# Performance work log

Hardware: AMD Instinct MI355X
Metric: run time of the kernel (lower is better)

## Reference

```python
import jax, jax.numpy as jnp
import numpy as np

N_ENT = 50000
N_REL = 200
N_EDGE = 1_000_000
D = 64


def setup_inputs() -> dict:
    key = jax.random.key(0)
    ks = jax.random.split(key, 12)
    src = jax.random.randint(ks[0], (N_EDGE,), 0, N_ENT)
    rel = jax.random.randint(ks[1], (N_EDGE,), 0, N_REL)
    dst = jax.random.randint(ks[2], (N_EDGE,), 0, N_ENT)
    triples = jnp.stack([src, rel, dst], axis=1).astype(jnp.int64)  # [E,3]
    s = 1.0 / np.sqrt(D)
    return {
        "emb_e": jax.random.normal(ks[3], (N_ENT, D), jnp.float32) * s,
        "re_att": jax.random.normal(ks[4], (N_REL,), jnp.float32) * 0.1,
        "W1": jax.random.normal(ks[5], (D, D), jnp.float32) * s,
        "W2": jax.random.normal(ks[6], (D, D), jnp.float32) * s,
        "W3": jax.random.normal(ks[7], (D, D), jnp.float32) * s,
        "u": jax.random.normal(ks[8], (3 * D,), jnp.float32) * s,
        "en_weight": jax.random.normal(ks[9], (D, D), jnp.float32) * s,
        "re_weight": jax.random.normal(ks[10], (D, D), jnp.float32) * s,
        "re_spec": jax.random.normal(ks[11], (D,), jnp.float32) * s,
        "triples": triples,
    }


def _forward(emb_e, re_att, W1, W2, W3, u, en_weight, re_weight, re_spec, triples):
    src = triples[:, 0]
    rel = triples[:, 1]
    dst = triples[:, 2]
    n = emb_e.shape[0]

    def wgc(x, W):
        # relation-weighted message passing: out[s] += w[r] * x[d]
        msg = jax.ops.segment_sum(x[dst] * re_att[rel][:, None], src, num_segments=n)
        return jnp.tanh((x + msg) @ W)

    x = wgc(emb_e, W1)
    x = wgc(x, W2)
    x = wgc(x, W3)

    # GAT-style edge scores: e = LeakyReLU(u . [W_en h_i ; W_re r_spec ; W_en h_j])
    d = x.shape[1]
    hs = x @ en_weight.T                       # [N,d] = (en_weight @ h)^T rows
    z_src = hs @ u[:d]                         # [N]
    z_dst = hs @ u[2 * d:]                     # [N]
    z_mid = u[d:2 * d] @ (re_weight @ re_spec)  # scalar, same for every edge
    scores = jax.nn.leaky_relu(z_src[src] + z_mid + z_dst[dst], 0.01)  # [E]

    # softmax normalized over ALL triples (global denominator, per source code)
    alpha = jax.nn.softmax(scores)

    # out[src] += alpha_e * x[dst]
    out = jax.ops.segment_sum(alpha[:, None] * x[dst], src, num_segments=n)
    return out


def reference(emb_e, re_att, W1, W2, W3, u, en_weight, re_weight, re_spec, triples):
    return _forward(emb_e, re_att, W1, W2, W3, u, en_weight, re_weight, re_spec, triples)
```

## Files before the change

### kernel.cpp

```cpp
#include <hip/hip_runtime.h>
#include <math.h>

#define N_ENT  50000
#define N_REL  200
#define N_EDGE 1000000
#define CHUNK  196
#define ECH    7813
#define NRNG   6250

#define WS_MISC   0
#define WS_ZSUM   128
#define WS_ZMID   192
#define WS_A      256
#define WS_B      512
#define WS_BSUM   0x000E0000
#define WS_BBASE  0x000F0000
#define WS_COUNTS 0x00100000
#define WS_OFFS   0x00140000
#define WS_ZSRC   0x00180000
#define WS_ZDST   0x001C0000
#define WS_SNODE  0x00200000
#define WS_EPK    0x00240000
#define WS_PACKED 0x00640000
#define WS_SRCS   0x00A40000
#define WS_RANK   0x00E40000
#define WS_XB1    0x00A40000
#define WS_XB0    0x01240000

__device__ __forceinline__ float bflo(unsigned u) { return __uint_as_float(u << 16); }
__device__ __forceinline__ float bfhi(unsigned u) { return __uint_as_float(u & 0xffff0000u); }
__device__ __forceinline__ unsigned short f2bf(float f) {
  unsigned u = __float_as_uint(f);
  unsigned r = ((u >> 16) & 1u) + 0x7fffu;
  return (unsigned short)((u + r) >> 16);
}
__device__ __forceinline__ float lanebc(float v, int k) {
  return __uint_as_float((unsigned)__builtin_amdgcn_readlane((int)__float_as_uint(v), k));
}
__device__ __forceinline__ float fast_tanh(float x) {
  float ex = __expf(2.f * x);
  return 1.f - __fdividef(2.f, ex + 1.f);
}
__device__ __forceinline__ void fma8(float* acc, float wt, uint4 q) {
  acc[0] += wt * bflo(q.x); acc[1] += wt * bfhi(q.x);
  acc[2] += wt * bflo(q.y); acc[3] += wt * bfhi(q.y);
  acc[4] += wt * bflo(q.z); acc[5] += wt * bfhi(q.z);
  acc[6] += wt * bflo(q.w); acc[7] += wt * bfhi(q.w);
}

__global__ void k_init(const void* tri, int* counts, int* misc, double* zsum) {
  int i = blockIdx.x * blockDim.x + threadIdx.x;
  if (i < N_ENT) counts[i] = 0;
  if (blockIdx.x == 0 && threadIdx.x < 64) {
    int l = threadIdx.x;
    int z = ((const int*)tri)[2 * l + 1];
    unsigned long long m = __ballot(z == 0);
    if (l == 0) { misc[0] = (m == ~0ull) ? 1 : 0; *zsum = 0.0; }
  }
}

__global__ void k_conv(const float* __restrict__ x, unsigned short* __restrict__ xb) {
  int i = blockIdx.x * blockDim.x + threadIdx.x;
  if (i >= N_ENT * 16) return;
  float4 v = ((const float4*)x)[i];
  ushort4 o;
  o.x = f2bf(v.x); o.y = f2bf(v.y); o.z = f2bf(v.z); o.w = f2bf(v.w);
  ((ushort4*)xb)[i] = o;
}

__global__ void k_decode(const void* tri, int* __restrict__ counts,
                         int* __restrict__ srcs, unsigned* __restrict__ packed,
                         int* __restrict__ rank, const int* misc) {
  int is64 = misc[0];
  int stride = gridDim.x * blockDim.x;
  if (is64) {
    const long long* t = (const long long*)tri;
    for (int e = blockIdx.x * blockDim.x + threadIdx.x; e < N_EDGE; e += stride) {
      int s = (int)t[3 * e], r = (int)t[3 * e + 1], d = (int)t[3 * e + 2];
      srcs[e] = s;
      packed[e] = ((unsigned)r << 16) | (unsigned)d;
      rank[e] = atomicAdd(&counts[s], 1);
    }
  } else {
    const int* t = (const int*)tri;
    for (int e = blockIdx.x * blockDim.x + threadIdx.x; e < N_EDGE; e += stride) {
      int s = t[3 * e], r = t[3 * e + 1], d = t[3 * e + 2];
      srcs[e] = s;
      packed[e] = ((unsigned)r << 16) | (unsigned)d;
      rank[e] = atomicAdd(&counts[s], 1);
    }
  }
}

__global__ void k_scanA(const int* __restrict__ counts, int* __restrict__ bsum) {
  __shared__ int sm[4];
  int t = threadIdx.x;
  int i = blockIdx.x * CHUNK + t;
  int v = (t < CHUNK && i < N_ENT) ? counts[i] : 0;
  for (int o = 32; o; o >>= 1) v += __shfl_down(v, o);
  if ((t & 63) == 0) sm[t >> 6] = v;
  __syncthreads();
  if (t == 0) bsum[blockIdx.x] = sm[0] + sm[1] + sm[2] + sm[3];
}

__global__ void k_scanB(const int* __restrict__ bsum, int* __restrict__ bbase, int* __restrict__ offs) {
  __shared__ int sm[256];
  int t = threadIdx.x;
  int v = bsum[t];
  sm[t] = v;
  __syncthreads();
  for (int d = 1; d < 256; d <<= 1) {
    int x = (t >= d) ? sm[t - d] : 0;
    __syncthreads();
    sm[t] += x;
    __syncthreads();
  }
  bbase[t] = sm[t] - v;
  if (t == 255) offs[N_ENT] = sm[255];
}

__global__ void k_scanC(const int* __restrict__ counts, const int* __restrict__ bbase,
                        int* __restrict__ offs) {
  __shared__ int sm[256];
  int t = threadIdx.x;
  int i = blockIdx.x * CHUNK + t;
  int v = (t < CHUNK && i < N_ENT) ? counts[i] : 0;
  sm[t] = v;
  __syncthreads();
  for (int d = 1; d < 256; d <<= 1) {
    int x = (t >= d) ? sm[t - d] : 0;
    __syncthreads();
    sm[t] += x;
    __syncthreads();
  }
  if (t < CHUNK && i < N_ENT)
    offs[i] = bbase[blockIdx.x] + sm[t] - v;
}

__global__ void k_scatter(const int* __restrict__ srcs, const int* __restrict__ rank,
                          const unsigned* __restrict__ packed, const int* __restrict__ offs,
                          unsigned* __restrict__ epk) {
  int q = blockIdx.x >> 3, x = blockIdx.x & 7;
  int lo = q * ECH, hi = lo + ECH;
  if (hi > N_EDGE) hi = N_EDGE;
  for (int e = lo + threadIdx.x; e < hi; e += 256) {
    int s = srcs[e];
    if (s / NRNG == x)
      epk[offs[s] + rank[e]] = packed[e];
  }
}

__global__ void k_pre(const float* u, const float* enw, const float* rew, const float* rsp,
                      float* a, float* b, float* zmid) {
  int k = threadIdx.x;
  float aa = 0.f, bb = 0.f;
  for (int j = 0; j < 64; j++) {
    float w = enw[j * 64 + k];
    aa += u[j] * w;
    bb += u[128 + j] * w;
  }
  a[k] = aa; b[k] = bb;
  float t = 0.f;
  for (int c = 0; c < 64; c++) t += rew[k * 64 + c] * rsp[c];
  t *= u[64 + k];
  for (int o = 32; o; o >>= 1) t += __shfl_down(t, o);
  if (k == 0) *zmid = t;
}

template <int EPI>
__global__ void __launch_bounds__(256) k_wgc(
    const unsigned short* __restrict__ xb, const float* __restrict__ W,
    const int* __restrict__ offs, const unsigned* __restrict__ epk,
    const float* __restrict__ re_att, unsigned short* __restrict__ yb,
    const float* __restrict__ a, const float* __restrict__ b,
    float* __restrict__ zsrc, float* __restrict__ zdst) {
  __shared__ float s_att[N_REL];
  for (int t = threadIdx.x; t < N_REL; t += 256) s_att[t] = re_att[t];
  __syncthreads();
  int wid = (blockIdx.x * blockDim.x + threadIdx.x) >> 6;
  int lane = threadIdx.x & 63;
  if (wid >= N_ENT) return;
  int node = wid;
  int g = lane >> 3, c8 = (lane & 7) * 8;
  int e0 = offs[node], e1 = offs[node + 1];
  float acc[8] = {0.f, 0.f, 0.f, 0.f, 0.f, 0.f, 0.f, 0.f};
  {
    uint4 q = *(const uint4*)(xb + (size_t)node * 64 + c8);
    fma8(acc, (g == 0) ? 1.f : 0.f, q);
  }
  for (int e = e0; e < e1; e += 16) {
    int ia = e + g, ib = ia + 8;
    bool va = ia < e1, vb = ib < e1;
    unsigned pa = epk[va ? ia : e0];
    unsigned pb = epk[vb ? ib : e0];
    float wa = va ? s_att[pa >> 16] : 0.f;
    float wb = vb ? s_att[pb >> 16] : 0.f;
    uint4 qa = *(const uint4*)(xb + (size_t)(pa & 0xffffu) * 64 + c8);
    uint4 qb = *(const uint4*)(xb + (size_t)(pb & 0xffffu) * 64 + c8);
    fma8(acc, wa, qa);
    fma8(acc, wb, qb);
  }
#pragma unroll
  for (int off = 8; off <= 32; off <<= 1)
#pragma unroll
    for (int c = 0; c < 8; c++) acc[c] += __shfl_xor(acc[c], off);
  float o = 0.f;
#pragma unroll
  for (int j = 0; j < 8; j++)
#pragma unroll
    for (int c = 0; c < 8; c++)
      o += lanebc(acc[c], j) * W[(j * 8 + c) * 64 + lane];
  float yv = fast_tanh(o);
  yb[(size_t)node * 64 + lane] = f2bf(yv);
  if (EPI) {
    float za = yv * a[lane], zb = yv * b[lane];
    for (int s = 32; s; s >>= 1) { za += __shfl_down(za, s); zb += __shfl_down(zb, s); }
    if (lane == 0) { zsrc[node] = za; zdst[node] = zb; }
  }
}

__global__ void __launch_bounds__(256) k_out(
    const unsigned short* __restrict__ xb, const int* __restrict__ offs,
    const unsigned* __restrict__ epk, const float* __restrict__ zs,
    const float* __restrict__ zd, const float* zmid,
    float* __restrict__ out, float* __restrict__ snode) {
  int wid = (blockIdx.x * blockDim.x + threadIdx.x) >> 6;
  int lane = threadIdx.x & 63;
  if (wid >= N_ENT) return;
  int node = wid;
  int g = lane >> 3, c8 = (lane & 7) * 8;
  float zi = zs[node] + *zmid;
  float acc[8] = {0.f, 0.f, 0.f, 0.f, 0.f, 0.f, 0.f, 0.f};
  float s0 = 0.f;
  int e0 = offs[node], e1 = offs[node + 1];
  for (int e = e0; e < e1; e += 16) {
    int ia = e + g, ib = ia + 8;
    bool va = ia < e1, vb = ib < e1;
    unsigned pa = epk[va ? ia : e0];
    unsigned pb = epk[vb ? ib : e0];
    int da = pa & 0xffffu, db = pb & 0xffffu;
    float ca = zi + zd[da];
    float cb = zi + zd[db];
    ca = ca >= 0.f ? ca : 0.01f * ca;
    cb = cb >= 0.f ? cb : 0.01f * cb;
    float wa = va ? __expf(ca) : 0.f;
    float wb = vb ? __expf(cb) : 0.f;
    uint4 qa = *(const uint4*)(xb + (size_t)da * 64 + c8);
    uint4 qb = *(const uint4*)(xb + (size_t)db * 64 + c8);
    fma8(acc, wa, qa);
    fma8(acc, wb, qb);
    s0 += wa + wb;
  }
#pragma unroll
  for (int off = 8; off <= 32; off <<= 1) {
#pragma unroll
    for (int c = 0; c < 8; c++) acc[c] += __shfl_xor(acc[c], off);
    s0 += __shfl_xor(s0, off);
  }
  if (lane < 8) {
    float4* p = (float4*)(out + (size_t)node * 64 + lane * 8);
    p[0] = make_float4(acc[0], acc[1], acc[2], acc[3]);
    p[1] = make_float4(acc[4], acc[5], acc[6], acc[7]);
  }
  if (lane == 0) snode[node] = s0;
}

__global__ void k_red(const float* __restrict__ snode, double* zsum) {
  int stride = gridDim.x * blockDim.x;
  double s = 0.0;
  for (int i = blockIdx.x * blockDim.x + threadIdx.x; i < N_ENT; i += stride)
    s += (double)snode[i];
  for (int o = 32; o; o >>= 1) s += __shfl_down(s, o);
  __shared__ double ws_[4];
  if ((threadIdx.x & 63) == 0) ws_[threadIdx.x >> 6] = s;
  __syncthreads();
  if (threadIdx.x == 0)
    atomicAdd(zsum, ws_[0] + ws_[1] + ws_[2] + ws_[3]);
}

__global__ void k_norm(float* __restrict__ out, const double* zsum) {
  int i = blockIdx.x * blockDim.x + threadIdx.x;
  if (i >= N_ENT * 16) return;
  float invZ = (float)(1.0 / *zsum);
  float4 v = ((float4*)out)[i];
  v.x *= invZ; v.y *= invZ; v.z *= invZ; v.w *= invZ;
  ((float4*)out)[i] = v;
}

extern "C" void kernel_launch(void* const* d_in, const int* in_sizes, int n_in,
                              void* d_out, int out_size, void* d_ws, size_t ws_size,
                              hipStream_t stream) {
  const float* emb   = (const float*)d_in[0];
  const float* reatt = (const float*)d_in[1];
  const float* W1    = (const float*)d_in[2];
  const float* W2    = (const float*)d_in[3];
  const float* W3    = (const float*)d_in[4];
  const float* u     = (const float*)d_in[5];
  const float* enw   = (const float*)d_in[6];
  const float* rew   = (const float*)d_in[7];
  const float* rsp   = (const float*)d_in[8];
  const void*  tri   = d_in[9];

  char* ws = (char*)d_ws;
  int*            misc   = (int*)(ws + WS_MISC);
  double*         zsum   = (double*)(ws + WS_ZSUM);
  float*          zmid   = (float*)(ws + WS_ZMID);
  float*          a      = (float*)(ws + WS_A);
  float*          b      = (float*)(ws + WS_B);
  int*            bsum   = (int*)(ws + WS_BSUM);
  int*            bbase  = (int*)(ws + WS_BBASE);
  int*            counts = (int*)(ws + WS_COUNTS);
  int*            offs   = (int*)(ws + WS_OFFS);
  float*          zsrc   = (float*)(ws + WS_ZSRC);
  float*          zdst   = (float*)(ws + WS_ZDST);
  float*          snode  = (float*)(ws + WS_SNODE);
  unsigned*       epk    = (unsigned*)(ws + WS_EPK);
  unsigned*       packed = (unsigned*)(ws + WS_PACKED);
  int*            srcs   = (int*)(ws + WS_SRCS);
  int*            rank   = (int*)(ws + WS_RANK);
  unsigned short* xb0    = (unsigned short*)(ws + WS_XB0);
  unsigned short* xb1    = (unsigned short*)(ws + WS_XB1);
  float*          out    = (float*)d_out;

  k_init<<<196, 256, 0, stream>>>(tri, counts, misc, zsum);
  k_conv<<<3125, 256, 0, stream>>>(emb, xb0);
  k_decode<<<1024, 256, 0, stream>>>(tri, counts, srcs, packed, rank, misc);
  k_scanA<<<256, 256, 0, stream>>>(counts, bsum);
  k_scanB<<<1, 256, 0, stream>>>(bsum, bbase, offs);
  k_scanC<<<256, 256, 0, stream>>>(counts, bbase, offs);
  k_scatter<<<1024, 256, 0, stream>>>(srcs, rank, packed, offs, epk);
  k_pre<<<1, 64, 0, stream>>>(u, enw, rew, rsp, a, b, zmid);

  int nb = (N_ENT * 64 + 255) / 256;
  k_wgc<0><<<nb, 256, 0, stream>>>(xb0, W1, offs, epk, reatt, xb1, nullptr, nullptr, nullptr, nullptr);
  k_wgc<0><<<nb, 256, 0, stream>>>(xb1, W2, offs, epk, reatt, xb0, nullptr, nullptr, nullptr, nullptr);
  k_wgc<1><<<nb, 256, 0, stream>>>(xb0, W3, offs, epk, reatt, xb1, a, b, zsrc, zdst);

  k_out<<<nb, 256, 0, stream>>>(xb1, offs, epk, zsrc, zdst, zmid, out, snode);
  k_red<<<196, 256, 0, stream>>>(snode, zsum);
  k_norm<<<3125, 256, 0, stream>>>(out, zsum);
}
```

Measured before the change: 247.2 us.

## Replicate per-source counters eightfold to cut atomic contention in CSR build

Edge decoding now spreads its per-source atomic counters across 8 replicas chosen by block index, and packs src, replica and rank into one word. This reduces the three per-edge arrays to two. A new merge kernel turns the replica counts into per-replica base offsets and totals, which feed the existing scan. The scatter then uses offs + rbase + rank to place each edge. The aim is less atomic contention and less intermediate memory traffic, at the cost of an extra kernel, 8x larger counter init, and a rank field limited to 13 bits.

```diff
diff --git a/kernel.cpp b/kernel.cpp
--- a/kernel.cpp
+++ b/kernel.cpp
@@ -11,19 +11,20 @@
 #define WS_MISC   0
 #define WS_ZSUM   128
 #define WS_ZMID   192
-#define WS_A      256
-#define WS_B      512
+#define WS_AV     256
+#define WS_BV     512
 #define WS_BSUM   0x000E0000
 #define WS_BBASE  0x000F0000
-#define WS_COUNTS 0x00100000
-#define WS_OFFS   0x00140000
-#define WS_ZSRC   0x00180000
-#define WS_ZDST   0x001C0000
-#define WS_SNODE  0x00200000
-#define WS_EPK    0x00240000
-#define WS_PACKED 0x00640000
-#define WS_SRCS   0x00A40000
-#define WS_RANK   0x00E40000
+#define WS_CNT8   0x00100000
+#define WS_RBASE  0x00300000
+#define WS_TOT    0x00500000
+#define WS_OFFS   0x00540000
+#define WS_ZSRC   0x00580000
+#define WS_ZDST   0x005C0000
+#define WS_SNODE  0x00600000
+#define WS_EPK    0x00640000
+#define WS_EA     0x00A40000
+#define WS_EB     0x00E40000
 #define WS_XB1    0x00A40000
 #define WS_XB0    0x01240000
 
@@ -48,9 +49,9 @@
   acc[6] += wt * bflo(q.w); acc[7] += wt * bfhi(q.w);
 }
 
-__global__ void k_init(const void* tri, int* counts, int* misc, double* zsum) {
+__global__ void k_init(const void* tri, int* cnt8, int* misc, double* zsum) {
   int i = blockIdx.x * blockDim.x + threadIdx.x;
-  if (i < N_ENT) counts[i] = 0;
+  if (i < 8 * N_ENT) cnt8[i] = 0;
   if (blockIdx.x == 0 && threadIdx.x < 64) {
     int l = threadIdx.x;
     int z = ((const int*)tri)[2 * l + 1];
@@ -68,28 +69,42 @@
   ((ushort4*)xb)[i] = o;
 }
 
-__global__ void k_decode(const void* tri, int* __restrict__ counts,
-                         int* __restrict__ srcs, unsigned* __restrict__ packed,
-                         int* __restrict__ rank, const int* misc) {
+__global__ void k_decode(const void* tri, int* __restrict__ cnt8,
+                         unsigned* __restrict__ ea, unsigned* __restrict__ eb,
+                         const int* misc) {
   int is64 = misc[0];
+  int rep = blockIdx.x & 7;
   int stride = gridDim.x * blockDim.x;
   if (is64) {
     const long long* t = (const long long*)tri;
     for (int e = blockIdx.x * blockDim.x + threadIdx.x; e < N_EDGE; e += stride) {
       int s = (int)t[3 * e], r = (int)t[3 * e + 1], d = (int)t[3 * e + 2];
-      srcs[e] = s;
-      packed[e] = ((unsigned)r << 16) | (unsigned)d;
-      rank[e] = atomicAdd(&counts[s], 1);
+      int rk = atomicAdd(&cnt8[rep * N_ENT + s], 1);
+      ea[e] = ((unsigned)s << 16) | ((unsigned)rep << 13) | (unsigned)rk;
+      eb[e] = ((unsigned)r << 16) | (unsigned)d;
     }
   } else {
     const int* t = (const int*)tri;
     for (int e = blockIdx.x * blockDim.x + threadIdx.x; e < N_EDGE; e += stride) {
       int s = t[3 * e], r = t[3 * e + 1], d = t[3 * e + 2];
-      srcs[e] = s;
-      packed[e] = ((unsigned)r << 16) | (unsigned)d;
-      rank[e] = atomicAdd(&counts[s], 1);
+      int rk = atomicAdd(&cnt8[rep * N_ENT + s], 1);
+      ea[e] = ((unsigned)s << 16) | ((unsigned)rep << 13) | (unsigned)rk;
+      eb[e] = ((unsigned)r << 16) | (unsigned)d;
     }
   }
+}
+
+__global__ void k_merge(const int* __restrict__ cnt8, int* __restrict__ rbase,
+                        int* __restrict__ tot) {
+  int s = blockIdx.x * blockDim.x + threadIdx.x;
+  if (s >= N_ENT) return;
+  int run = 0;
+#pragma unroll
+  for (int rep = 0; rep < 8; rep++) {
+    rbase[rep * N_ENT + s] = run;
+    run += cnt8[rep * N_ENT + s];
+  }
+  tot[s] = run;
 }
 
 __global__ void k_scanA(const int* __restrict__ counts, int* __restrict__ bsum) {
@@ -137,16 +152,20 @@
     offs[i] = bbase[blockIdx.x] + sm[t] - v;
 }
 
-__global__ void k_scatter(const int* __restrict__ srcs, const int* __restrict__ rank,
-                          const unsigned* __restrict__ packed, const int* __restrict__ offs,
+__global__ void k_scatter(const unsigned* __restrict__ ea, const unsigned* __restrict__ eb,
+                          const int* __restrict__ offs, const int* __restrict__ rbase,
                           unsigned* __restrict__ epk) {
   int q = blockIdx.x >> 3, x = blockIdx.x & 7;
   int lo = q * ECH, hi = lo + ECH;
   if (hi > N_EDGE) hi = N_EDGE;
   for (int e = lo + threadIdx.x; e < hi; e += 256) {
-    int s = srcs[e];
-    if (s / NRNG == x)
-      epk[offs[s] + rank[e]] = packed[e];
+    unsigned a = ea[e];
+    int s = a >> 16;
+    if (s / NRNG == x) {
+      int rep = (a >> 13) & 7;
+      int rk = a & 8191;
+      epk[offs[s] + rbase[rep * N_ENT + s] + rk] = eb[e];
+    }
   }
 }
 
@@ -305,36 +324,38 @@
   int*            misc   = (int*)(ws + WS_MISC);
   double*         zsum   = (double*)(ws + WS_ZSUM);
   float*          zmid   = (float*)(ws + WS_ZMID);
-  float*          a      = (float*)(ws + WS_A);
-  float*          b      = (float*)(ws + WS_B);
+  float*          av     = (float*)(ws + WS_AV);
+  float*          bv     = (float*)(ws + WS_BV);
   int*            bsum   = (int*)(ws + WS_BSUM);
   int*            bbase  = (int*)(ws + WS_BBASE);
-  int*            counts = (int*)(ws + WS_COUNTS);
+  int*            cnt8   = (int*)(ws + WS_CNT8);
+  int*            rbase  = (int*)(ws + WS_RBASE);
+  int*            tot    = (int*)(ws + WS_TOT);
   int*            offs   = (int*)(ws + WS_OFFS);
   float*          zsrc   = (float*)(ws + WS_ZSRC);
   float*          zdst   = (float*)(ws + WS_ZDST);
   float*          snode  = (float*)(ws + WS_SNODE);
   unsigned*       epk    = (unsigned*)(ws + WS_EPK);
-  unsigned*       packed = (unsigned*)(ws + WS_PACKED);
-  int*            srcs   = (int*)(ws + WS_SRCS);
-  int*            rank   = (int*)(ws + WS_RANK);
+  unsigned*       ea     = (unsigned*)(ws + WS_EA);
+  unsigned*       eb     = (unsigned*)(ws + WS_EB);
   unsigned short* xb0    = (unsigned short*)(ws + WS_XB0);
   unsigned short* xb1    = (unsigned short*)(ws + WS_XB1);
   float*          out    = (float*)d_out;
 
-  k_init<<<196, 256, 0, stream>>>(tri, counts, misc, zsum);
+  k_init<<<1563, 256, 0, stream>>>(tri, cnt8, misc, zsum);
   k_conv<<<3125, 256, 0, stream>>>(emb, xb0);
-  k_decode<<<1024, 256, 0, stream>>>(tri, counts, srcs, packed, rank, misc);
-  k_scanA<<<256, 256, 0, stream>>>(counts, bsum);
+  k_decode<<<4096, 256, 0, stream>>>(tri, cnt8, ea, eb, misc);
+  k_merge<<<196, 256, 0, stream>>>(cnt8, rbase, tot);
+  k_scanA<<<256, 256, 0, stream>>>(tot, bsum);
   k_scanB<<<1, 256, 0, stream>>>(bsum, bbase, offs);
-  k_scanC<<<256, 256, 0, stream>>>(counts, bbase, offs);
-  k_scatter<<<1024, 256, 0, stream>>>(srcs, rank, packed, offs, epk);
-  k_pre<<<1, 64, 0, stream>>>(u, enw, rew, rsp, a, b, zmid);
+  k_scanC<<<256, 256, 0, stream>>>(tot, bbase, offs);
+  k_scatter<<<1024, 256, 0, stream>>>(ea, eb, offs, rbase, epk);
+  k_pre<<<1, 64, 0, stream>>>(u, enw, rew, rsp, av, bv, zmid);
 
   int nb = (N_ENT * 64 + 255) / 256;
   k_wgc<0><<<nb, 256, 0, stream>>>(xb0, W1, offs, epk, reatt, xb1, nullptr, nullptr, nullptr, nullptr);
   k_wgc<0><<<nb, 256, 0, stream>>>(xb1, W2, offs, epk, reatt, xb0, nullptr, nullptr, nullptr, nullptr);
-  k_wgc<1><<<nb, 256, 0, stream>>>(xb0, W3, offs, epk, reatt, xb1, a, b, zsrc, zdst);
+  k_wgc<1><<<nb, 256, 0, stream>>>(xb0, W3, offs, epk, reatt, xb1, av, bv, zsrc, zdst);
 
   k_out<<<nb, 256, 0, stream>>>(xb1, offs, epk, zsrc, zdst, zmid, out, snode);
   k_red<<<196, 256, 0, stream>>>(snode, zsum);
```

New measurement: 243.8 us. About the same (-1.4%).
